# Performance work log

Measured on AMD Instinct MI355X. Metric: run time of the kernel, lower is better.

## Reference

```python
import jax, jax.numpy as jnp
import numpy as np

N = 100000      # nodes
E = 1000000     # edges per neighborhood
C_IN = 64
C_OUT = 64
EPS = 1e-5


def _pna_aggregate(row, col, msg, W, b, n):
    """PNA-style multi-stat neighborhood aggregation: gather neighbor messages,
    compute sum/mean/max/std per target node, combine with a linear layer."""
    g = msg[col]  # [E, F] gathered source messages
    ones = jnp.ones((row.shape[0],), msg.dtype)
    cnt = jax.ops.segment_sum(ones, row, num_segments=n)          # [N]
    s = jax.ops.segment_sum(g, row, num_segments=n)               # [N, F]
    sq = jax.ops.segment_sum(g * g, row, num_segments=n)          # [N, F]
    c = jnp.maximum(cnt, 1.0)[:, None]
    mean = s / c
    var = jnp.maximum(sq / c - mean * mean, 0.0)
    std = jnp.sqrt(var + EPS)
    mx = jax.ops.segment_max(g, row, num_segments=n)
    mx = jnp.where(cnt[:, None] > 0, mx, 0.0)                     # empty segments -> 0
    feats = jnp.concatenate([s, mean, mx, std], axis=-1)          # [N, 4F]
    return feats @ W + b


def _layer_norm(x, gamma, beta):
    mu = jnp.mean(x, axis=-1, keepdims=True)
    var = jnp.mean((x - mu) ** 2, axis=-1, keepdims=True)
    return (x - mu) * jax.lax.rsqrt(var + EPS) * gamma + beta


def setup_inputs() -> dict:
    key = jax.random.key(0)
    ks = jax.random.split(key, 12)
    gain = 1.414
    xav = gain * np.sqrt(2.0 / (C_IN + C_OUT))
    xav_p = np.sqrt(2.0 / (4 * C_OUT + C_OUT))
    return {
        "x_source": jax.random.normal(ks[0], (N, C_IN), jnp.float32),
        "weight": jax.random.uniform(ks[1], (C_IN, C_OUT), jnp.float32, -xav, xav),
        "weight2": jax.random.uniform(ks[2], (C_IN, C_OUT), jnp.float32, -xav, xav),
        "pna_w1": jax.random.uniform(ks[3], (4 * C_OUT, C_OUT), jnp.float32, -xav_p, xav_p),
        "pna_b1": jnp.zeros((C_OUT,), jnp.float32),
        "pna_w2": jax.random.uniform(ks[4], (4 * C_OUT, C_OUT), jnp.float32, -xav_p, xav_p),
        "pna_b2": jnp.zeros((C_OUT,), jnp.float32),
        "gamma": jnp.ones((C_OUT,), jnp.float32),
        "beta": jnp.zeros((C_OUT,), jnp.float32),
        "nb_row": jnp.sort(jax.random.randint(ks[5], (E,), 0, N, jnp.int32)),
        "nb_col": jax.random.randint(ks[6], (E,), 0, N, jnp.int32),
        "cci_row": jnp.sort(jax.random.randint(ks[7], (E,), 0, N, jnp.int32)),
        "cci_col": jax.random.randint(ks[8], (E,), 0, N, jnp.int32),
    }


def reference(x_source, weight, weight2, pna_w1, pna_b1, pna_w2, pna_b2,
              gamma, beta, nb_row, nb_col, cci_row, cci_col):
    # linear transforms
    message = x_source @ weight     # [N, F]
    message2 = x_source @ weight2   # [N, F]
    # two sparse PNA aggregations (neighborhood and cci), then add
    m1 = _pna_aggregate(nb_row, nb_col, message, pna_w1, pna_b1, N)
    m2 = _pna_aggregate(cci_row, cci_col, message2, pna_w2, pna_b2, N)
    result = m1 + m2
    # update: activation (relu) + layer norm
    return _layer_norm(jax.nn.relu(result), gamma, beta)
```

## Files before the change

kernel.cpp:

```cpp
#include <hip/hip_runtime.h>
#include <math.h>

#define EPS 1e-5f

typedef __attribute__((ext_vector_type(8))) short bf16x8;
typedef __attribute__((ext_vector_type(4))) float f32x4;

__device__ __forceinline__ ushort f2bf(float f) {
    union { float f; unsigned u; } v; v.f = f;
    unsigned u = v.u;
    return (ushort)((u + 0x7fffu + ((u >> 16) & 1u)) >> 16);
}
__device__ __forceinline__ float bf2f(ushort h) {
    union { unsigned u; float f; } v; v.u = ((unsigned)h) << 16;
    return v.f;
}
__device__ __forceinline__ float bflo(uint u) {
    union { unsigned a; float f; } v; v.a = u << 16;
    return v.f;
}
__device__ __forceinline__ float bfhi(uint u) {
    union { unsigned a; float f; } v; v.a = u & 0xffff0000u;
    return v.f;
}
__device__ __forceinline__ uint cvtpk(float lo, float hi) {
    uint r;
    asm("v_cvt_pk_bf16_f32 %0, %1, %2" : "=v"(r) : "v"(lo), "v"(hi));
    return r;
}
__device__ __forceinline__ float fast_rcp(float x) {
    float r; asm("v_rcp_f32 %0, %1" : "=v"(r) : "v"(x)); return r;
}
__device__ __forceinline__ float fast_rsq(float x) {
    float r; asm("v_rsq_f32 %0, %1" : "=v"(r) : "v"(x)); return r;
}

__global__ __launch_bounds__(256) void prep_all(
    const int* __restrict__ row1, int* __restrict__ ptr1, int E1,
    const int* __restrict__ row2, int* __restrict__ ptr2, int E2,
    const int* __restrict__ col1, int* __restrict__ col1p,
    const int* __restrict__ col2, int* __restrict__ col2p,
    const float* __restrict__ pw1, const float* __restrict__ pw2,
    const float* __restrict__ w1, const float* __restrict__ w2,
    ushort* __restrict__ wt1, ushort* __restrict__ wt2,
    ushort* __restrict__ wtl1, ushort* __restrict__ wtl2,
    ushort* __restrict__ m1z, ushort* __restrict__ m2z,
    int n, int B1, int B2, int C1, int C2)
{
    const int b = blockIdx.x;
    if (b < B1 + B2) {
        const int* row = (b < B1) ? row1 : row2;
        int* ptr = (b < B1) ? ptr1 : ptr2;
        const int E = (b < B1) ? E1 : E2;
        const int bb = (b < B1) ? b : b - B1;
        int e = bb * 256 + threadIdx.x;
        if (e >= E) return;
        int r = row[e];
        if (e == 0) {
            for (int j = 0; j <= r; ++j) ptr[j] = 0;
        }
        int rn = (e == E - 1) ? n : row[e + 1];
        for (int j = r + 1; j <= rn; ++j) ptr[j] = e + 1;
    } else if (b < B1 + B2 + C1 + C2) {
        const bool g1 = (b < B1 + B2 + C1);
        const int* src = g1 ? col1 : col2;
        int* dst = g1 ? col1p : col2p;
        const int E = g1 ? E1 : E2;
        const int bb = g1 ? (b - B1 - B2) : (b - B1 - B2 - C1);
        int e = bb * 256 + threadIdx.x;
        if (e < E) dst[e] = src[e];
        else if (e < E + 16) dst[e] = n;
    } else {
        int idx = (b - B1 - B2 - C1 - C2) * 256 + threadIdx.x;
        if (idx < 16384) {
            int k = idx >> 6, j = idx & 63;
            wt1[j * 256 + k] = f2bf(pw1[idx]);
            wt2[j * 256 + k] = f2bf(pw2[idx]);
        }
        if (idx < 4096) {
            int k = idx >> 6, j = idx & 63;
            wtl1[j * 64 + k] = f2bf(w1[idx]);
            wtl2[j * 64 + k] = f2bf(w2[idx]);
        }
        if (idx < 64) {
            m1z[idx] = 0;
            m2z[idx] = 0;
        }
    }
}

__global__ __launch_bounds__(512) void linear_mfma(const float* __restrict__ x,
                                                   const ushort* __restrict__ wtl1,
                                                   const ushort* __restrict__ wtl2,
                                                   ushort* __restrict__ m1,
                                                   ushort* __restrict__ m2, int n)
{
    const int tid = threadIdx.x, wv = tid >> 6, lane = tid & 63;
    const int r = lane & 15, c = lane >> 4;
    const int nodebase = blockIdx.x * 128 + wv * 16;
    const int anode = nodebase + r;

    bf16x8 a[2];
#pragma unroll
    for (int kt = 0; kt < 2; ++kt) {
        float4 lo = {0.f, 0.f, 0.f, 0.f}, hi = {0.f, 0.f, 0.f, 0.f};
        if (anode < n) {
            lo = *(const float4*)&x[(size_t)anode * 64 + kt * 32 + c * 8];
            hi = *(const float4*)&x[(size_t)anode * 64 + kt * 32 + c * 8 + 4];
        }
        ushort t[8] = {f2bf(lo.x), f2bf(lo.y), f2bf(lo.z), f2bf(lo.w),
                       f2bf(hi.x), f2bf(hi.y), f2bf(hi.z), f2bf(hi.w)};
        a[kt] = *(const bf16x8*)t;
    }

    f32x4 acc1[4] = {{0.f,0.f,0.f,0.f},{0.f,0.f,0.f,0.f},
                     {0.f,0.f,0.f,0.f},{0.f,0.f,0.f,0.f}};
    f32x4 acc2[4] = {{0.f,0.f,0.f,0.f},{0.f,0.f,0.f,0.f},
                     {0.f,0.f,0.f,0.f},{0.f,0.f,0.f,0.f}};
#pragma unroll
    for (int kt = 0; kt < 2; ++kt) {
#pragma unroll
        for (int nt = 0; nt < 4; ++nt) {
            bf16x8 b1 = *(const bf16x8*)&wtl1[(nt * 16 + r) * 64 + kt * 32 + c * 8];
            bf16x8 b2 = *(const bf16x8*)&wtl2[(nt * 16 + r) * 64 + kt * 32 + c * 8];
            acc1[nt] = __builtin_amdgcn_mfma_f32_16x16x32_bf16(a[kt], b1, acc1[nt], 0, 0, 0);
            acc2[nt] = __builtin_amdgcn_mfma_f32_16x16x32_bf16(a[kt], b2, acc2[nt], 0, 0, 0);
        }
    }

#pragma unroll
    for (int e = 0; e < 4; ++e) {
        const int i = nodebase + c * 4 + e;
        if (i < n) {
#pragma unroll
            for (int nt = 0; nt < 4; ++nt) {
                m1[(size_t)i * 64 + nt * 16 + r] = f2bf(acc1[nt][e]);
                m2[(size_t)i * 64 + nt * 16 + r] = f2bf(acc2[nt][e]);
            }
        }
    }
}

__device__ __forceinline__ void agg_pass(const ushort* __restrict__ msg,
                                         const int* __restrict__ colp,
                                         const ushort* __restrict__ wt,
                                         int rpv, ushort (*stw)[256],
                                         f32x4 acc[4],
                                         int nodebase, int lane, int n, int E)
{
    const int grp = lane >> 4;
    const int fq  = lane & 15;
    const uint fqb = (uint)fq << 3;
    const char* msgc = (const char*)msg;

    for (int qd = 0; qd < 4; ++qd) {
        const int b0 = __builtin_amdgcn_readlane(rpv, 4 * qd);
        const int b1 = __builtin_amdgcn_readlane(rpv, 4 * qd + 1);
        const int b2 = __builtin_amdgcn_readlane(rpv, 4 * qd + 2);
        const int b3 = __builtin_amdgcn_readlane(rpv, 4 * qd + 3);
        const int b4 = __builtin_amdgcn_readlane(rpv, 4 * qd + 4);
        int e0 = (grp & 1) ? b1 : b0;
        int eA = (grp & 1) ? b3 : b2;
        e0 = (grp & 2) ? eA : e0;
        int e1 = (grp & 1) ? b2 : b1;
        int eB = (grp & 1) ? b4 : b3;
        e1 = (grp & 2) ? eB : e1;
        const int cnt = e1 - e0;

        float s0 = 0.f, s1 = 0.f, s2 = 0.f, s3 = 0.f;
        float q0 = 0.f, q1 = 0.f, q2 = 0.f, q3 = 0.f;
        float m0 = -INFINITY, m1v = -INFINITY, m2v = -INFINITY, m3 = -INFINITY;

        for (int off = 0; ; off += 16) {
            const int* cwin = colp + e0 + off;
            uint cv[16];
#pragma unroll
            for (int t = 0; t < 16; ++t) cv[t] = ((const uint*)cwin)[t];

            uint2 gv[16];
#pragma unroll
            for (int t = 0; t < 16; ++t) {
                const bool valid = (off + t) < cnt;
                const uint row = valid ? cv[t] : (uint)n;
                gv[t] = *(const uint2*)(msgc + (((size_t)row << 7) + fqb));
            }
#pragma unroll
            for (int t = 0; t < 16; ++t) {
                const bool valid = (off + t) < cnt;
                const float f0 = bflo(gv[t].x), f1 = bfhi(gv[t].x);
                const float f2 = bflo(gv[t].y), f3 = bfhi(gv[t].y);
                s0 += f0; q0 = fmaf(f0, f0, q0);
                s1 += f1; q1 = fmaf(f1, f1, q1);
                s2 += f2; q2 = fmaf(f2, f2, q2);
                s3 += f3; q3 = fmaf(f3, f3, q3);
                m0  = fmaxf(m0,  valid ? f0 : -INFINITY);
                m1v = fmaxf(m1v, valid ? f1 : -INFINITY);
                m2v = fmaxf(m2v, valid ? f2 : -INFINITY);
                m3  = fmaxf(m3,  valid ? f3 : -INFINITY);
            }
            if (!__any(cnt > off + 16)) break;
        }

        const float cf = (cnt > 0) ? (float)cnt : 1.f;
        const float inv = fast_rcp(cf);
        const float mean0 = s0 * inv, mean1 = s1 * inv;
        const float mean2 = s2 * inv, mean3 = s3 * inv;
        float v0 = q0 * inv - mean0 * mean0; if (v0 < 0.f) v0 = 0.f;
        float v1 = q1 * inv - mean1 * mean1; if (v1 < 0.f) v1 = 0.f;
        float v2 = q2 * inv - mean2 * mean2; if (v2 < 0.f) v2 = 0.f;
        float v3 = q3 * inv - mean3 * mean3; if (v3 < 0.f) v3 = 0.f;
        const float sd0 = (v0 + EPS) * fast_rsq(v0 + EPS);
        const float sd1 = (v1 + EPS) * fast_rsq(v1 + EPS);
        const float sd2 = (v2 + EPS) * fast_rsq(v2 + EPS);
        const float sd3 = (v3 + EPS) * fast_rsq(v3 + EPS);
        if (cnt == 0) { m0 = 0.f; m1v = 0.f; m2v = 0.f; m3 = 0.f; }

        const int nn = 4 * qd + grp;
        char* rowp = (char*)&stw[nn][0];
        const int sw = (nn & 7) << 4;
        uint2 w;
        w.x = cvtpk(s0, s1);       w.y = cvtpk(s2, s3);
        *(uint2*)(rowp + ((0   + (int)fqb) ^ sw)) = w;
        w.x = cvtpk(mean0, mean1); w.y = cvtpk(mean2, mean3);
        *(uint2*)(rowp + ((128 + (int)fqb) ^ sw)) = w;
        w.x = cvtpk(m0, m1v);      w.y = cvtpk(m2v, m3);
        *(uint2*)(rowp + ((256 + (int)fqb) ^ sw)) = w;
        w.x = cvtpk(sd0, sd1);     w.y = cvtpk(sd2, sd3);
        *(uint2*)(rowp + ((384 + (int)fqb) ^ sw)) = w;
    }

    const int r = lane & 15, c = lane >> 4;
    const char* arow = (const char*)&stw[r][0];
    const int asw = (r & 7) << 4;
#pragma unroll
    for (int kt = 0; kt < 8; ++kt) {
        bf16x8 a = *(const bf16x8*)(arow + ((kt * 64 + c * 16) ^ asw));
#pragma unroll
        for (int nt = 0; nt < 4; ++nt) {
            bf16x8 b = *(const bf16x8*)&wt[(nt * 16 + r) * 256 + kt * 32 + c * 8];
            acc[nt] = __builtin_amdgcn_mfma_f32_16x16x32_bf16(a, b, acc[nt], 0, 0, 0);
        }
    }
}

__global__ __launch_bounds__(128) void pna_pass1(
    const ushort* __restrict__ msg, const int* __restrict__ rptr,
    const int* __restrict__ colp, const ushort* __restrict__ wt,
    ushort* __restrict__ partial, int n, int E)
{
    __shared__ ushort st[2][16][256];
    const int tid = threadIdx.x;
    const int wv = tid >> 6, lane = tid & 63;
    const int nodebase = blockIdx.x * 32 + wv * 16;

    int rpidx = nodebase + (lane & 31);
    if (rpidx > n) rpidx = n;
    const int rpv = rptr[rpidx];

    f32x4 acc[4] = {{0.f,0.f,0.f,0.f},{0.f,0.f,0.f,0.f},
                    {0.f,0.f,0.f,0.f},{0.f,0.f,0.f,0.f}};

    agg_pass(msg, colp, wt, rpv, st[wv], acc, nodebase, lane, n, E);

    const int r = lane & 15, c = lane >> 4;
#pragma unroll
    for (int e = 0; e < 4; ++e) {
        const int i = nodebase + c * 4 + e;
        if (i < n) {
#pragma unroll
            for (int nt = 0; nt < 4; ++nt)
                partial[(size_t)i * 64 + nt * 16 + r] = f2bf(acc[nt][e]);
        }
    }
}

__global__ __launch_bounds__(128) void pna_pass2(
    const ushort* __restrict__ msg, const int* __restrict__ rptr,
    const int* __restrict__ colp, const ushort* __restrict__ wt,
    const float* __restrict__ b1, const float* __restrict__ b2,
    const float* __restrict__ gamma, const float* __restrict__ beta,
    const ushort* __restrict__ partial, float* __restrict__ out,
    int n, int E)
{
    __shared__ ushort st[2][16][256];
    const int tid = threadIdx.x;
    const int wv = tid >> 6, lane = tid & 63;
    const int nodebase = blockIdx.x * 32 + wv * 16;

    int rpidx = nodebase + (lane & 31);
    if (rpidx > n) rpidx = n;
    const int rpv = rptr[rpidx];

    f32x4 acc[4] = {{0.f,0.f,0.f,0.f},{0.f,0.f,0.f,0.f},
                    {0.f,0.f,0.f,0.f},{0.f,0.f,0.f,0.f}};

    agg_pass(msg, colp, wt, rpv, st[wv], acc, nodebase, lane, n, E);

    const int r = lane & 15, c = lane >> 4;
    float biasv[4], gmv[4], btv[4];
#pragma unroll
    for (int nt = 0; nt < 4; ++nt) {
        biasv[nt] = b1[nt * 16 + r] + b2[nt * 16 + r];
        gmv[nt] = gamma[nt * 16 + r];
        btv[nt] = beta[nt * 16 + r];
    }
#pragma unroll
    for (int e = 0; e < 4; ++e) {
        const int i = nodebase + c * 4 + e;
        float v[4];
        float sum = 0.f;
#pragma unroll
        for (int nt = 0; nt < 4; ++nt) {
            float t = 0.f;
            if (i < n)
                t = fmaxf(acc[nt][e] + biasv[nt] +
                          bf2f(partial[(size_t)i * 64 + nt * 16 + r]), 0.f);
            v[nt] = t;
            sum += t;
        }
        sum += __shfl_xor(sum, 1);
        sum += __shfl_xor(sum, 2);
        sum += __shfl_xor(sum, 4);
        sum += __shfl_xor(sum, 8);
        const float mu = sum * (1.f / 64.f);
        float sqs = 0.f;
#pragma unroll
        for (int nt = 0; nt < 4; ++nt) {
            float d = v[nt] - mu;
            sqs += d * d;
        }
        sqs += __shfl_xor(sqs, 1);
        sqs += __shfl_xor(sqs, 2);
        sqs += __shfl_xor(sqs, 4);
        sqs += __shfl_xor(sqs, 8);
        const float rs = rsqrtf(sqs * (1.f / 64.f) + EPS);
        if (i < n) {
#pragma unroll
            for (int nt = 0; nt < 4; ++nt)
                out[(size_t)i * 64 + nt * 16 + r] =
                    (v[nt] - mu) * rs * gmv[nt] + btv[nt];
        }
    }
}

extern "C" void kernel_launch(void* const* d_in, const int* in_sizes, int n_in,
                              void* d_out, int out_size, void* d_ws, size_t ws_size,
                              hipStream_t stream)
{
    const float* x     = (const float*)d_in[0];
    const float* w1    = (const float*)d_in[1];
    const float* w2    = (const float*)d_in[2];
    const float* pw1   = (const float*)d_in[3];
    const float* pb1   = (const float*)d_in[4];
    const float* pw2   = (const float*)d_in[5];
    const float* pb2   = (const float*)d_in[6];
    const float* gamma = (const float*)d_in[7];
    const float* beta  = (const float*)d_in[8];
    const int* nb_row  = (const int*)d_in[9];
    const int* nb_col  = (const int*)d_in[10];
    const int* cci_row = (const int*)d_in[11];
    const int* cci_col = (const int*)d_in[12];

    const int n  = in_sizes[0] / 64;
    const int E1 = in_sizes[9];
    const int E2 = in_sizes[11];

    char* p = (char*)d_ws;
    ushort* msg1 = (ushort*)p;  p += (size_t)(n + 1) * 64 * sizeof(ushort);
    ushort* msg2 = (ushort*)p;  p += (size_t)(n + 1) * 64 * sizeof(ushort);
    int* ptr1 = (int*)p;        p += (size_t)(n + 1) * sizeof(int);
    int* ptr2 = (int*)p;        p += (size_t)(n + 1) * sizeof(int);
    p = (char*)(((uintptr_t)p + 63) & ~(uintptr_t)63);
    ushort* wt1 = (ushort*)p;   p += 16384 * sizeof(ushort);
    ushort* wt2 = (ushort*)p;   p += 16384 * sizeof(ushort);
    ushort* wtl1 = (ushort*)p;  p += 4096 * sizeof(ushort);
    ushort* wtl2 = (ushort*)p;  p += 4096 * sizeof(ushort);
    ushort* partial = (ushort*)p; p += (size_t)n * 64 * sizeof(ushort);
    p = (char*)(((uintptr_t)p + 63) & ~(uintptr_t)63);
    int* col1p = (int*)p;       p += (size_t)(E1 + 16) * sizeof(int);
    int* col2p = (int*)p;
    float* outf = (float*)d_out;

    const int B1 = (E1 + 255) / 256, B2 = (E2 + 255) / 256;
    const int C1 = (E1 + 16 + 255) / 256, C2 = (E2 + 16 + 255) / 256;
    prep_all<<<B1 + B2 + C1 + C2 + 64, 256, 0, stream>>>(
        nb_row, ptr1, E1, cci_row, ptr2, E2,
        nb_col, col1p, cci_col, col2p,
        pw1, pw2, w1, w2, wt1, wt2, wtl1, wtl2,
        msg1 + (size_t)n * 64, msg2 + (size_t)n * 64, n, B1, B2, C1, C2);
    linear_mfma<<<(n + 127) / 128, 512, 0, stream>>>(x, wtl1, wtl2, msg1, msg2, n);

    const int grid = (n + 31) / 32;
    pna_pass1<<<grid, 128, 0, stream>>>(msg1, ptr1, col1p, wt1, partial, n, E1);
    pna_pass2<<<grid, 128, 0, stream>>>(msg2, ptr2, col2p, wt2,
                                        pb1, pb2, gamma, beta, partial, outf, n, E2);
}
```

Before: 135.2 us.

## Stage column indices in LDS and double-buffer gather batches across node quads

Each wave now loads its 16 nodes' column indices into a shared-memory buffer with one coalesced pass, then reads them from LDS instead of issuing 16 scalar-address global loads per group. The per-quad gather loop is split into issue and consume phases with two register buffers, so the gathers for the next node quad are in flight while the current quad's statistics are reduced. Tails longer than 16 edges fall back to a separate 8-wide loop that reads indices from global memory. This raises register pressure (two 16-entry uint2 buffers) and adds LDS, which may reduce occupancy.

```diff
diff --git a/kernel.cpp b/kernel.cpp
--- a/kernel.cpp
+++ b/kernel.cpp
@@ -2,6 +2,7 @@
 #include <math.h>
 
 #define EPS 1e-5f
+#define COLCAP 512
 
 typedef __attribute__((ext_vector_type(8))) short bf16x8;
 typedef __attribute__((ext_vector_type(4))) float f32x4;
@@ -145,6 +146,7 @@
                                          const int* __restrict__ colp,
                                          const ushort* __restrict__ wt,
                                          int rpv, ushort (*stw)[256],
+                                         int* __restrict__ colbuf,
                                          f32x4 acc[4],
                                          int nodebase, int lane, int n, int E)
 {
@@ -153,7 +155,16 @@
     const uint fqb = (uint)fq << 3;
     const char* msgc = (const char*)msg;
 
-    for (int qd = 0; qd < 4; ++qd) {
+    const int e0w = __builtin_amdgcn_readlane(rpv, 0);
+    const int e1w = __builtin_amdgcn_readlane(rpv, 16);
+    int tot = e1w - e0w;
+    if (tot > COLCAP) tot = COLCAP;
+    for (int t = lane; t < tot; t += 64) colbuf[t] = colp[e0w + t];
+
+    uint2 gvA[16], gvB[16];
+    int e0A = 0, cntA = 0, e0B = 0, cntB = 0;
+
+    auto ISSUE = [&](int qd, uint2 (&gv)[16], int& e0o, int& cnto) {
         const int b0 = __builtin_amdgcn_readlane(rpv, 4 * qd);
         const int b1 = __builtin_amdgcn_readlane(rpv, 4 * qd + 1);
         const int b2 = __builtin_amdgcn_readlane(rpv, 4 * qd + 2);
@@ -166,42 +177,72 @@
         int eB = (grp & 1) ? b4 : b3;
         e1 = (grp & 2) ? eB : e1;
         const int cnt = e1 - e0;
-
+        e0o = e0; cnto = cnt;
+        const int lb = e0 - e0w;
+        uint cv[16];
+        if (lb + 16 <= tot) {
+#pragma unroll
+            for (int t = 0; t < 16; ++t) cv[t] = (uint)colbuf[lb + t];
+        } else {
+#pragma unroll
+            for (int t = 0; t < 16; ++t) {
+                int ci = e0 + t; if (ci > E - 1) ci = E - 1;
+                cv[t] = (uint)colp[ci];
+            }
+        }
+#pragma unroll
+        for (int t = 0; t < 16; ++t) {
+            const uint row = (t < cnt) ? cv[t] : (uint)n;
+            gv[t] = *(const uint2*)(msgc + (((size_t)row << 7) + fqb));
+        }
+    };
+
+    auto CONSUME = [&](int qd, uint2 (&gv)[16], int e0v, int cntv) {
         float s0 = 0.f, s1 = 0.f, s2 = 0.f, s3 = 0.f;
         float q0 = 0.f, q1 = 0.f, q2 = 0.f, q3 = 0.f;
         float m0 = -INFINITY, m1v = -INFINITY, m2v = -INFINITY, m3 = -INFINITY;
-
-        for (int off = 0; ; off += 16) {
-            const int* cwin = colp + e0 + off;
-            uint cv[16];
-#pragma unroll
-            for (int t = 0; t < 16; ++t) cv[t] = ((const uint*)cwin)[t];
-
-            uint2 gv[16];
-#pragma unroll
-            for (int t = 0; t < 16; ++t) {
-                const bool valid = (off + t) < cnt;
-                const uint row = valid ? cv[t] : (uint)n;
-                gv[t] = *(const uint2*)(msgc + (((size_t)row << 7) + fqb));
+#pragma unroll
+        for (int t = 0; t < 16; ++t) {
+            const bool valid = t < cntv;
+            const float f0 = bflo(gv[t].x), f1 = bfhi(gv[t].x);
+            const float f2 = bflo(gv[t].y), f3 = bfhi(gv[t].y);
+            s0 += f0; q0 = fmaf(f0, f0, q0);
+            s1 += f1; q1 = fmaf(f1, f1, q1);
+            s2 += f2; q2 = fmaf(f2, f2, q2);
+            s3 += f3; q3 = fmaf(f3, f3, q3);
+            m0  = fmaxf(m0,  valid ? f0 : -INFINITY);
+            m1v = fmaxf(m1v, valid ? f1 : -INFINITY);
+            m2v = fmaxf(m2v, valid ? f2 : -INFINITY);
+            m3  = fmaxf(m3,  valid ? f3 : -INFINITY);
+        }
+        if (__any(cntv > 16)) {
+            const int e1_ = e0v + cntv;
+            for (int off = 16; __any(e0v + off < e1_); off += 8) {
+                uint2 gx[8];
+#pragma unroll
+                for (int t = 0; t < 8; ++t) {
+                    int ci = e0v + off + t; if (ci > E - 1) ci = E - 1;
+                    const bool valid = (off + t) < cntv;
+                    const uint row = valid ? (uint)colp[ci] : (uint)n;
+                    gx[t] = *(const uint2*)(msgc + (((size_t)row << 7) + fqb));
+                }
+#pragma unroll
+                for (int t = 0; t < 8; ++t) {
+                    const bool valid = (off + t) < cntv;
+                    const float f0 = bflo(gx[t].x), f1 = bfhi(gx[t].x);
+                    const float f2 = bflo(gx[t].y), f3 = bfhi(gx[t].y);
+                    s0 += f0; q0 = fmaf(f0, f0, q0);
+                    s1 += f1; q1 = fmaf(f1, f1, q1);
+                    s2 += f2; q2 = fmaf(f2, f2, q2);
+                    s3 += f3; q3 = fmaf(f3, f3, q3);
+                    m0  = fmaxf(m0,  valid ? f0 : -INFINITY);
+                    m1v = fmaxf(m1v, valid ? f1 : -INFINITY);
+                    m2v = fmaxf(m2v, valid ? f2 : -INFINITY);
+                    m3  = fmaxf(m3,  valid ? f3 : -INFINITY);
+                }
             }
-#pragma unroll
-            for (int t = 0; t < 16; ++t) {
-                const bool valid = (off + t) < cnt;
-                const float f0 = bflo(gv[t].x), f1 = bfhi(gv[t].x);
-                const float f2 = bflo(gv[t].y), f3 = bfhi(gv[t].y);
-                s0 += f0; q0 = fmaf(f0, f0, q0);
-                s1 += f1; q1 = fmaf(f1, f1, q1);
-                s2 += f2; q2 = fmaf(f2, f2, q2);
-                s3 += f3; q3 = fmaf(f3, f3, q3);
-                m0  = fmaxf(m0,  valid ? f0 : -INFINITY);
-                m1v = fmaxf(m1v, valid ? f1 : -INFINITY);
-                m2v = fmaxf(m2v, valid ? f2 : -INFINITY);
-                m3  = fmaxf(m3,  valid ? f3 : -INFINITY);
-            }
-            if (!__any(cnt > off + 16)) break;
-        }
-
-        const float cf = (cnt > 0) ? (float)cnt : 1.f;
+        }
+        const float cf = (cntv > 0) ? (float)cntv : 1.f;
         const float inv = fast_rcp(cf);
         const float mean0 = s0 * inv, mean1 = s1 * inv;
         const float mean2 = s2 * inv, mean3 = s3 * inv;
@@ -213,7 +254,7 @@
         const float sd1 = (v1 + EPS) * fast_rsq(v1 + EPS);
         const float sd2 = (v2 + EPS) * fast_rsq(v2 + EPS);
         const float sd3 = (v3 + EPS) * fast_rsq(v3 + EPS);
-        if (cnt == 0) { m0 = 0.f; m1v = 0.f; m2v = 0.f; m3 = 0.f; }
+        if (cntv == 0) { m0 = 0.f; m1v = 0.f; m2v = 0.f; m3 = 0.f; }
 
         const int nn = 4 * qd + grp;
         char* rowp = (char*)&stw[nn][0];
@@ -227,7 +268,16 @@
         *(uint2*)(rowp + ((256 + (int)fqb) ^ sw)) = w;
         w.x = cvtpk(sd0, sd1);     w.y = cvtpk(sd2, sd3);
         *(uint2*)(rowp + ((384 + (int)fqb) ^ sw)) = w;
-    }
+    };
+
+    ISSUE(0, gvA, e0A, cntA);
+    ISSUE(1, gvB, e0B, cntB);
+    CONSUME(0, gvA, e0A, cntA);
+    ISSUE(2, gvA, e0A, cntA);
+    CONSUME(1, gvB, e0B, cntB);
+    ISSUE(3, gvB, e0B, cntB);
+    CONSUME(2, gvA, e0A, cntA);
+    CONSUME(3, gvB, e0B, cntB);
 
     const int r = lane & 15, c = lane >> 4;
     const char* arow = (const char*)&stw[r][0];
@@ -249,6 +299,7 @@
     ushort* __restrict__ partial, int n, int E)
 {
     __shared__ ushort st[2][16][256];
+    __shared__ int colb[2][COLCAP];
     const int tid = threadIdx.x;
     const int wv = tid >> 6, lane = tid & 63;
     const int nodebase = blockIdx.x * 32 + wv * 16;
@@ -260,7 +311,7 @@
     f32x4 acc[4] = {{0.f,0.f,0.f,0.f},{0.f,0.f,0.f,0.f},
                     {0.f,0.f,0.f,0.f},{0.f,0.f,0.f,0.f}};
 
-    agg_pass(msg, colp, wt, rpv, st[wv], acc, nodebase, lane, n, E);
+    agg_pass(msg, colp, wt, rpv, st[wv], colb[wv], acc, nodebase, lane, n, E);
 
     const int r = lane & 15, c = lane >> 4;
 #pragma unroll
@@ -283,6 +334,7 @@
     int n, int E)
 {
     __shared__ ushort st[2][16][256];
+    __shared__ int colb[2][COLCAP];
     const int tid = threadIdx.x;
     const int wv = tid >> 6, lane = tid & 63;
     const int nodebase = blockIdx.x * 32 + wv * 16;
@@ -294,7 +346,7 @@
     f32x4 acc[4] = {{0.f,0.f,0.f,0.f},{0.f,0.f,0.f,0.f},
                     {0.f,0.f,0.f,0.f},{0.f,0.f,0.f,0.f}};
 
-    agg_pass(msg, colp, wt, rpv, st[wv], acc, nodebase, lane, n, E);
+    agg_pass(msg, colp, wt, rpv, st[wv], colb[wv], acc, nodebase, lane, n, E);
 
     const int r = lane & 15, c = lane >> 4;
     float biasv[4], gmv[4], btv[4];
```

Measured after the change: 147.6 us. +9.2%, slower.
